# Kernel optimization log

Hardware: AMD Instinct MI355X
Metric: run time of the kernel (lower is better)

The kernel has to match this reference:

```python
import jax, jax.numpy as jnp
import numpy as np

E = 64      # encoding_size (hard-coded in MatchingNetwork)
K = 5       # processing_steps


def _cell(x, h, c, Wih, Whh, bih, bhh):
    # PyTorch LSTMCell: gates ordered i, f, g, o
    z = x @ Wih.T + h @ Whh.T + bih + bhh
    i, f, g, o = jnp.split(z, 4, axis=-1)
    c2 = jax.nn.sigmoid(f) * c + jax.nn.sigmoid(i) * jnp.tanh(g)
    h2 = jax.nn.sigmoid(o) * jnp.tanh(c2)
    return h2, c2


def _lstm_seq(xs, Wih, Whh, bih, bhh, reverse=False):
    # xs: [B, S, E] -> per-step hidden states [B, S, E]
    B = xs.shape[0]
    xs_t = jnp.swapaxes(xs, 0, 1)  # [S, B, E]
    if reverse:
        xs_t = xs_t[::-1]
    h0 = jnp.zeros((B, Wih.shape[0] // 4), xs.dtype)

    def step(carry, x_t):
        h, c = carry
        h2, c2 = _cell(x_t, h, c, Wih, Whh, bih, bhh)
        return (h2, c2), h2

    _, hs = jax.lax.scan(step, (h0, h0), xs_t)
    if reverse:
        hs = hs[::-1]
    return jnp.swapaxes(hs, 0, 1)


def setup_inputs() -> dict:
    key = jax.random.key(0)
    ks = jax.random.split(key, 16)
    B, N, k, T, L, V = 64, 20, 10, 128, 40, 32000
    support_tokens = jax.random.randint(ks[0], (B, N, k, L), 0, V)
    target_tokens = jax.random.randint(ks[1], (B, T, L), 0, V)
    emb = jax.random.normal(ks[2], (V, E), jnp.float32) * 0.1
    emb = emb.at[0].set(0.0)  # padding_idx row
    s = 1.0 / np.sqrt(E)

    def lstm_params(k1, k2, k3, k4):
        return (jax.random.uniform(k1, (4 * E, E), jnp.float32, -s, s),
                jax.random.uniform(k2, (4 * E, E), jnp.float32, -s, s),
                jax.random.uniform(k3, (4 * E,), jnp.float32, -s, s),
                jax.random.uniform(k4, (4 * E,), jnp.float32, -s, s))

    f_Wih, f_Whh, f_bih, f_bhh = lstm_params(ks[3], ks[4], ks[5], ks[6])
    gf_Wih, gf_Whh, gf_bih, gf_bhh = lstm_params(ks[7], ks[8], ks[9], ks[10])
    gb_Wih, gb_Whh, gb_bih, gb_bhh = lstm_params(ks[11], ks[12], ks[13], ks[14])
    return {
        'support_tokens': support_tokens, 'target_tokens': target_tokens,
        'emb': emb,
        'f_Wih': f_Wih, 'f_Whh': f_Whh, 'f_bih': f_bih, 'f_bhh': f_bhh,
        'gf_Wih': gf_Wih, 'gf_Whh': gf_Whh, 'gf_bih': gf_bih, 'gf_bhh': gf_bhh,
        'gb_Wih': gb_Wih, 'gb_Whh': gb_Whh, 'gb_bih': gb_bih, 'gb_bhh': gb_bhh,
    }


def reference(support_tokens, target_tokens, emb,
              f_Wih, f_Whh, f_bih, f_bhh,
              gf_Wih, gf_Whh, gf_bih, gf_bhh,
              gb_Wih, gb_Whh, gb_bih, gb_bhh):
    B, N, kk, L = support_tokens.shape
    T = target_tokens.shape[1]

    # EncodingLayer: embedding lookup + sum-pool over sentence length
    sup_enc = emb[support_tokens].sum(axis=3)   # [B, N, k, E]
    tgt_enc = emb[target_tokens].sum(axis=2)    # [B, T, E]

    # GLayer: bidirectional LSTM over flattened support, sum dirs + residual
    flat = sup_enc.reshape(B, N * kk, E)
    hf = _lstm_seq(flat, gf_Wih, gf_Whh, gf_bih, gf_bhh, reverse=False)
    hb = _lstm_seq(flat, gb_Wih, gb_Whh, gb_bih, gb_bhh, reverse=True)
    sup_emb = (hf + hb).reshape(B, N, kk, E) + sup_enc  # [B, N, k, E]

    # FLayer: K-step attention LSTM over targets
    x = tgt_enc.reshape(B * T, E)
    h = jnp.zeros_like(x)
    c = jnp.zeros_like(x)
    r = jnp.zeros_like(x)
    for _ in range(K):
        h = h + r
        h_next, c = _cell(x, h, c, f_Wih, f_Whh, f_bih, f_bhh)
        h_next = h_next + x
        scores = jnp.einsum('bte,bnke->btnk', h.reshape(B, T, E), sup_emb)
        att = jax.nn.softmax(scores.reshape(B, T, N * kk), axis=2).reshape(B, T, N, kk)
        r = jnp.einsum('btnk,bnke->bte', att, sup_emb).reshape(B * T, E)
        h = h_next
    tgt_emb = h.reshape(B, T, E)

    # Cosine-similarity attention over support set (softmax over N*k)
    num = jnp.einsum('bte,bnke->btnk', tgt_emb, sup_emb)
    tn = jnp.linalg.norm(tgt_emb, axis=-1)          # [B, T]
    sn = jnp.linalg.norm(sup_emb, axis=-1)          # [B, N, k]
    sims = num / jnp.maximum(tn[:, :, None, None] * sn[:, None, :, :], 1e-8)
    attention = jax.nn.softmax(sims.reshape(B, T, N * kk), axis=2).reshape(B, T, N, kk)
    return attention
```

## Files before the change

kernel.cpp:

```cpp
#include <hip/hip_runtime.h>

#define Bn   64
#define Tn   128
#define NKn  200
#define En   64
#define Ln   40

__device__ __forceinline__ float sigm_f(float x){ return 1.0f/(1.0f+__expf(-x)); }
__device__ __forceinline__ float tanh_f(float x){ float e=__expf(2.0f*x); return 1.0f-2.0f/(e+1.0f); }
__device__ __forceinline__ float rdl(float v, int ln){
  return __uint_as_float(__builtin_amdgcn_readlane(__float_as_uint(v), (unsigned)ln));
}

__global__ __launch_bounds__(256) void embed_all(const int* __restrict__ sup,
                                                 const int* __restrict__ tgt,
                                                 const float* __restrict__ emb,
                                                 float* __restrict__ sup_enc,
                                                 float* __restrict__ tgt_enc){
  int tid = threadIdx.x;
  int gr  = blockIdx.x*16 + (tid>>4);
  int e4  = tid & 15;
  const int* tr; float* out;
  if (gr < 12800){ tr = sup + (size_t)gr*Ln;        out = sup_enc + (size_t)gr*64; }
  else           { int r2=gr-12800; tr = tgt + (size_t)r2*Ln; out = tgt_enc + (size_t)r2*64; }
  float4 acc = {0.f,0.f,0.f,0.f};
  #pragma unroll 4
  for (int t=0;t<Ln;t++){
    int tok = tr[t];
    float4 v = ((const float4*)emb)[(size_t)tok*16 + e4];
    acc.x+=v.x; acc.y+=v.y; acc.z+=v.z; acc.w+=v.w;
  }
  ((float4*)out)[e4] = acc;
}

__global__ __launch_bounds__(256,1) void gemm_sup2(const float* __restrict__ x,
                                                   const float* __restrict__ Wa, const float* __restrict__ Wb,
                                                   const float* __restrict__ ba1,const float* __restrict__ ba2,
                                                   const float* __restrict__ bb1,const float* __restrict__ bb2,
                                                   float* __restrict__ outa, float* __restrict__ outb){
  int tid=threadIdx.x, l=tid&63, w=tid>>6;
  int g=tid;
  int m0 = blockIdx.x*16;
  __shared__ __attribute__((aligned(16))) float xs[16*64];
  #pragma unroll
  for(int q=0;q<4;q++){ int r=4*w+q; xs[r*64+l]=x[(size_t)(m0+r)*64+l]; }
  float wa[64], wb[64];
  {
    const float4* A4=(const float4*)(Wa + (size_t)g*64);
    const float4* B4=(const float4*)(Wb + (size_t)g*64);
    #pragma unroll
    for(int q=0;q<16;q++){
      float4 va=A4[q]; wa[4*q]=va.x; wa[4*q+1]=va.y; wa[4*q+2]=va.z; wa[4*q+3]=va.w;
      float4 vb=B4[q]; wb[4*q]=vb.x; wb[4*q+1]=vb.y; wb[4*q+2]=vb.z; wb[4*q+3]=vb.w;
    }
  }
  float biasa=ba1[g]+ba2[g], biasb=bb1[g]+bb2[g];
  __syncthreads();
  #pragma unroll
  for(int r=0;r<16;r++){
    const float4* x4=(const float4*)&xs[r*64];
    float a0=biasa,a1=0.f,b0=biasb,b1=0.f;
    #pragma unroll
    for(int kc=0;kc<16;kc++){
      float4 h4=x4[kc];
      a0=fmaf(wa[4*kc+0],h4.x,a0); b0=fmaf(wb[4*kc+0],h4.x,b0);
      a1=fmaf(wa[4*kc+1],h4.y,a1); b1=fmaf(wb[4*kc+1],h4.y,b1);
      a0=fmaf(wa[4*kc+2],h4.z,a0); b0=fmaf(wb[4*kc+2],h4.z,b0);
      a1=fmaf(wa[4*kc+3],h4.w,a1); b1=fmaf(wb[4*kc+3],h4.w,b1);
    }
    outa[(size_t)(m0+r)*256+g]=a0+a1;
    outb[(size_t)(m0+r)*256+g]=b0+b1;
  }
}

__global__ __launch_bounds__(512,2) void lstm_fb(const float* __restrict__ xg_f,
                                                 const float* __restrict__ xg_b,
                                                 const float* __restrict__ Whh_f,
                                                 const float* __restrict__ Whh_b,
                                                 float* __restrict__ hf,
                                                 float* __restrict__ hb){
  int tid=threadIdx.x, l=tid&63;
  int wl=(tid>>6)&3;
  int chain=tid>>8;
  int b=blockIdx.x;
  const float* xg = chain? xg_b : xg_f;
  const float* Whh= chain? Whh_b: Whh_f;
  float* out      = chain? hb : hf;
  int g=wl*64+l;
  float wr[64];
  {
    const float4* W4=(const float4*)(Whh+(size_t)g*64);
    #pragma unroll
    for(int q=0;q<16;q++){ float4 v=W4[q]; wr[4*q]=v.x; wr[4*q+1]=v.y; wr[4*q+2]=v.z; wr[4*q+3]=v.w; }
  }
  __shared__ float z_s[2][2][256];
  float h=0.f, c=0.f;
  const int tstart = chain?(NKn-1):0, dt = chain?-1:1;
  const float* xgb = xg + (size_t)b*NKn*256 + g;
  float xv0 = xgb[(size_t)tstart*256];
  float xv1 = xgb[(size_t)(tstart+dt)*256];
  for(int s=0;s<NKn;s++){
    int t=tstart+s*dt;
    float xnx=0.f;
    if (s+2<NKn) xnx = xgb[(size_t)(t+2*dt)*256];
    float a0=xv0,a1=0.f,a2=0.f,a3=0.f;
    #pragma unroll
    for(int q=0;q<16;q++){
      a0=fmaf(wr[4*q+0],rdl(h,4*q+0),a0);
      a1=fmaf(wr[4*q+1],rdl(h,4*q+1),a1);
      a2=fmaf(wr[4*q+2],rdl(h,4*q+2),a2);
      a3=fmaf(wr[4*q+3],rdl(h,4*q+3),a3);
    }
    int p=s&1;
    z_s[p][chain][g]=(a0+a1)+(a2+a3);
    __syncthreads();
    float zi=z_s[p][chain][l], zf=z_s[p][chain][64+l],
          zg2=z_s[p][chain][128+l], zo=z_s[p][chain][192+l];
    c = sigm_f(zf)*c + sigm_f(zi)*tanh_f(zg2);
    h = sigm_f(zo)*tanh_f(c);
    if(wl==0) out[((size_t)b*NKn+t)*64+l]=h;
    xv0=xv1; xv1=xnx;
  }
}

__global__ __launch_bounds__(256,2) void gemmz_combine(const float* __restrict__ tgt_enc,
                                                       const float* __restrict__ W,
                                                       const float* __restrict__ b1,
                                                       const float* __restrict__ b2,
                                                       float* __restrict__ zx,
                                                       const float* __restrict__ hf,
                                                       const float* __restrict__ hb,
                                                       const float* __restrict__ sup_enc,
                                                       float* __restrict__ semb,
                                                       float* __restrict__ sn){
  int tid=threadIdx.x, l=tid&63, w=tid>>6;
  int blk=blockIdx.x;
  if (blk < 512){
    int g=tid, m0=blk*16;
    __shared__ __attribute__((aligned(16))) float xs[16*64];
    #pragma unroll
    for(int q=0;q<4;q++){ int r=4*w+q; xs[r*64+l]=tgt_enc[(size_t)(m0+r)*64+l]; }
    float wr[64];
    const float4* W4=(const float4*)(W + (size_t)g*64);
    #pragma unroll
    for(int q=0;q<16;q++){ float4 v=W4[q]; wr[4*q]=v.x; wr[4*q+1]=v.y; wr[4*q+2]=v.z; wr[4*q+3]=v.w; }
    float bias=b1[g]+b2[g];
    __syncthreads();
    #pragma unroll
    for(int r=0;r<16;r++){
      const float4* x4=(const float4*)&xs[r*64];
      float a0=bias,a1=0.f,a2=0.f,a3=0.f;
      #pragma unroll
      for(int kc=0;kc<16;kc++){
        float4 h4=x4[kc];
        a0=fmaf(wr[4*kc+0],h4.x,a0);
        a1=fmaf(wr[4*kc+1],h4.y,a1);
        a2=fmaf(wr[4*kc+2],h4.z,a2);
        a3=fmaf(wr[4*kc+3],h4.w,a3);
      }
      zx[(size_t)(m0+r)*256+g]=(a0+a1)+(a2+a3);
    }
  } else {
    int m0=(blk-512)*16;
    #pragma unroll
    for(int q=0;q<4;q++){
      size_t m=(size_t)m0 + w*4 + q;
      float v = hf[m*64+l] + hb[m*64+l] + sup_enc[m*64+l];
      semb[m*64+l]=v;
      float s=v*v;
      #pragma unroll
      for (int o=32;o>0;o>>=1) s += __shfl_xor(s,o,64);
      if (l==0) sn[m]=sqrtf(s);
    }
  }
}

__global__ __launch_bounds__(256,1) void fused_K(const float* __restrict__ zx,
                                                 const float* __restrict__ Whh,
                                                 const float* __restrict__ x,
                                                 const float* __restrict__ semb,
                                                 const float* __restrict__ sn,
                                                 float* __restrict__ out){
  int tid=threadIdx.x, l=tid&63, w=tid>>6;
  int b=blockIdx.x>>3, t0=(blockIdx.x&7)*16;
  int m0=b*Tn+t0;
  int g=tid;
  bool valid = g<NKn;
  const float* sbase = semb + (size_t)b*NKn*64;
  __shared__ __attribute__((aligned(16))) float hu_s[16*64];
  __shared__ __attribute__((aligned(16))) float sbuf[16*256];
  __shared__ __attribute__((aligned(16))) float hn_s[16*64];
  __shared__ float wredA[64], wredB[64];
  float wr[64], s4f[64];
  {
    const float4* W4=(const float4*)(Whh+(size_t)g*64);
    #pragma unroll
    for(int q=0;q<16;q++){ float4 v=W4[q]; wr[4*q]=v.x; wr[4*q+1]=v.y; wr[4*q+2]=v.z; wr[4*q+3]=v.w; }
  }
  if(valid){
    const float4* sp=(const float4*)(sbase+(size_t)g*64);
    #pragma unroll
    for(int q=0;q<16;q++){ float4 v=sp[q]; s4f[4*q]=v.x; s4f[4*q+1]=v.y; s4f[4*q+2]=v.z; s4f[4*q+3]=v.w; }
  } else {
    #pragma unroll
    for(int q=0;q<64;q++) s4f[q]=0.f;
  }
  float zxr[16];
  #pragma unroll
  for(int r=0;r<16;r++) zxr[r]=zx[(size_t)(m0+r)*256+g];
  float xr[4];
  #pragma unroll
  for(int q=0;q<4;q++) xr[q]=x[(size_t)(m0+q*4+w)*64+l];
  float snr = valid ? sn[(size_t)b*NKn+g] : 1.f;
  float cq[4]={0.f,0.f,0.f,0.f};
  float scr[16], ex[16], mx[16];
  for(int k=0;k<5;k++){
    if(k==0){
      #pragma unroll
      for(int r=0;r<16;r++){ sbuf[r*256+g]=zxr[r]; scr[r]=0.f; }
    } else {
      #pragma unroll
      for(int r=0;r<16;r++){
        float z0=zxr[r], z1=0.f, sc0=0.f, sc1=0.f;
        const float4* h4p=(const float4*)&hu_s[r*64];
        #pragma unroll
        for(int kc=0;kc<16;kc++){
          float4 h4=h4p[kc];
          z0 =fmaf(wr[4*kc+0] ,h4.x,z0 ); sc0=fmaf(s4f[4*kc+0],h4.x,sc0);
          z1 =fmaf(wr[4*kc+1] ,h4.y,z1 ); sc1=fmaf(s4f[4*kc+1],h4.y,sc1);
          z0 =fmaf(wr[4*kc+2] ,h4.z,z0 ); sc0=fmaf(s4f[4*kc+2],h4.z,sc0);
          z1 =fmaf(wr[4*kc+3] ,h4.w,z1 ); sc1=fmaf(s4f[4*kc+3],h4.w,sc1);
        }
        sbuf[r*256+g]=z0+z1;
        scr[r]=sc0+sc1;
      }
    }
    __syncthreads();
    #pragma unroll
    for(int q=0;q<4;q++){
      int r=q*4+w;
      float zi=sbuf[r*256+l], zf=sbuf[r*256+64+l], zg=sbuf[r*256+128+l], zo=sbuf[r*256+192+l];
      float c=sigm_f(zf)*cq[q]+sigm_f(zi)*tanh_f(zg);
      cq[q]=c;
      hn_s[r*64+l]=sigm_f(zo)*tanh_f(c)+xr[q];
    }
    if(k<4){
      #pragma unroll
      for(int t=0;t<16;t++){
        float m = valid ? scr[t] : -1e30f;
        #pragma unroll
        for(int o=32;o>0;o>>=1) m=fmaxf(m,__shfl_xor(m,o,64));
        mx[t]=m;
      }
      if(l==0){
        #pragma unroll
        for(int t=0;t<16;t++) wredA[t*4+w]=mx[t];
      }
      __syncthreads();
      #pragma unroll
      for(int t=0;t<16;t++){
        const float4 m4=*(const float4*)&wredA[t*4];
        float gm=fmaxf(fmaxf(m4.x,m4.y),fmaxf(m4.z,m4.w));
        float e=valid?__expf(scr[t]-gm):0.f;
        ex[t]=e;
        float s=e;
        #pragma unroll
        for(int o=32;o>0;o>>=1) s+=__shfl_xor(s,o,64);
        mx[t]=s;
      }
      if(l==0){
        #pragma unroll
        for(int t=0;t<16;t++) wredB[t*4+w]=mx[t];
      }
      __syncthreads();
      #pragma unroll
      for(int t=0;t<16;t++){
        const float4 s4v=*(const float4*)&wredB[t*4];
        float tot=(s4v.x+s4v.y)+(s4v.z+s4v.w);
        ex[t]*=1.0f/tot;
      }
      if(valid){
        #pragma unroll
        for(int cg=0;cg<4;cg++)
          *(float4*)&sbuf[g*20+4*cg]=make_float4(ex[4*cg+0],ex[4*cg+1],ex[4*cg+2],ex[4*cg+3]);
      }
      __syncthreads();
      float r0=0.f,r1=0.f,r2=0.f,r3=0.f;
      #pragma unroll 8
      for(int j=0;j<NKn;j++){
        float4 a4=*(const float4*)&sbuf[j*20+w*4];
        float sv=sbase[(size_t)j*64+l];
        r0=fmaf(a4.x,sv,r0);
        r1=fmaf(a4.y,sv,r1);
        r2=fmaf(a4.z,sv,r2);
        r3=fmaf(a4.w,sv,r3);
      }
      int rb=w*4;
      hu_s[(rb+0)*64+l]=r0 + hn_s[(rb+0)*64+l];
      hu_s[(rb+1)*64+l]=r1 + hn_s[(rb+1)*64+l];
      hu_s[(rb+2)*64+l]=r2 + hn_s[(rb+2)*64+l];
      hu_s[(rb+3)*64+l]=r3 + hn_s[(rb+3)*64+l];
      __syncthreads();
    }
  }
  __syncthreads();
  float tnorm[16];
  #pragma unroll
  for(int t=0;t<16;t++){
    float v=hn_s[t*64+l];
    float s=v*v;
    #pragma unroll
    for(int o=32;o>0;o>>=1) s+=__shfl_xor(s,o,64);
    tnorm[t]=sqrtf(s);
  }
  #pragma unroll
  for(int t=0;t<16;t++){
    const float4* h4p=(const float4*)&hn_s[t*64];
    float a0=0.f,a1=0.f;
    #pragma unroll
    for(int kc=0;kc<16;kc++){
      float4 h4=h4p[kc];
      a0=fmaf(s4f[4*kc+0],h4.x,a0);
      a1=fmaf(s4f[4*kc+1],h4.y,a1);
      a0=fmaf(s4f[4*kc+2],h4.z,a0);
      a1=fmaf(s4f[4*kc+3],h4.w,a1);
    }
    scr[t]=(a0+a1) / fmaxf(tnorm[t]*snr,1e-8f);
  }
  #pragma unroll
  for(int t=0;t<16;t++){
    float m = valid ? scr[t] : -1e30f;
    #pragma unroll
    for(int o=32;o>0;o>>=1) m=fmaxf(m,__shfl_xor(m,o,64));
    mx[t]=m;
  }
  if(l==0){
    #pragma unroll
    for(int t=0;t<16;t++) wredA[t*4+w]=mx[t];
  }
  __syncthreads();
  #pragma unroll
  for(int t=0;t<16;t++){
    const float4 m4=*(const float4*)&wredA[t*4];
    float gm=fmaxf(fmaxf(m4.x,m4.y),fmaxf(m4.z,m4.w));
    float e=valid?__expf(scr[t]-gm):0.f;
    ex[t]=e;
    float s=e;
    #pragma unroll
    for(int o=32;o>0;o>>=1) s+=__shfl_xor(s,o,64);
    mx[t]=s;
  }
  if(l==0){
    #pragma unroll
    for(int t=0;t<16;t++) wredB[t*4+w]=mx[t];
  }
  __syncthreads();
  #pragma unroll
  for(int t=0;t<16;t++){
    const float4 s4v=*(const float4*)&wredB[t*4];
    float tot=(s4v.x+s4v.y)+(s4v.z+s4v.w);
    if(valid) out[((size_t)(m0+t))*NKn + g]=ex[t]*(1.0f/tot);
  }
}

extern "C" void kernel_launch(void* const* d_in, const int* in_sizes, int n_in,
                              void* d_out, int out_size, void* d_ws, size_t ws_size,
                              hipStream_t stream) {
  (void)in_sizes; (void)n_in; (void)out_size; (void)ws_size;
  const int*   sup_toks = (const int*)d_in[0];
  const int*   tgt_toks = (const int*)d_in[1];
  const float* emb      = (const float*)d_in[2];
  const float* f_Wih    = (const float*)d_in[3];
  const float* f_Whh    = (const float*)d_in[4];
  const float* f_bih    = (const float*)d_in[5];
  const float* f_bhh    = (const float*)d_in[6];
  const float* gf_Wih   = (const float*)d_in[7];
  const float* gf_Whh   = (const float*)d_in[8];
  const float* gf_bih   = (const float*)d_in[9];
  const float* gf_bhh   = (const float*)d_in[10];
  const float* gb_Wih   = (const float*)d_in[11];
  const float* gb_Whh   = (const float*)d_in[12];
  const float* gb_bih   = (const float*)d_in[13];
  const float* gb_bhh   = (const float*)d_in[14];

  float* ws = (float*)d_ws;
  float* sup_enc = ws;
  float* tgt_enc = sup_enc + 819200;
  float* bufA    = tgt_enc + 524288;
  float* bufB    = bufA    + 3276800;
  float* semb    = bufB    + 3276800;
  float* hb      = semb    + 819200;
  float* sn      = hb      + 819200;

  float* xg_f = bufA;
  float* xg_b = bufB;

  embed_all<<<1312,256,0,stream>>>(sup_toks, tgt_toks, emb, sup_enc, tgt_enc);
  gemm_sup2<<<800,256,0,stream>>>(sup_enc, gf_Wih, gb_Wih,
                                  gf_bih, gf_bhh, gb_bih, gb_bhh, xg_f, xg_b);
  lstm_fb<<<64,512,0,stream>>>(xg_f, xg_b, gf_Whh, gb_Whh, semb , hb);

  float* zx = bufA;

  gemmz_combine<<<1312,256,0,stream>>>(tgt_enc, f_Wih, f_bih, f_bhh, zx,
                                       semb, hb, sup_enc, semb, sn);

  fused_K<<<512,256,0,stream>>>(zx, f_Whh, tgt_enc, semb, sn, (float*)d_out);
}
```

Baseline: 422.2 us.

## Split bidirectional LSTM across blocks and K-dimension halves to shorten per-step chain

The recurrent support LSTM now uses 128 blocks, one per (direction, batch), instead of 64 blocks that each held both directions. Within a block, each gate row's 64-term recurrent dot product is split across two thread halves that combine partial sums through shared memory, which halves the serial FMA/readlane chain per step. Input-gate preloads are batched eight steps ahead, and hidden states are buffered in LDS and written out once at the end rather than every step. The cost is extra shared-memory traffic per step and a larger LDS footprint.

```diff
diff --git a/kernel.cpp b/kernel.cpp
--- a/kernel.cpp
+++ b/kernel.cpp
@@ -73,53 +73,69 @@
   }
 }
 
-__global__ __launch_bounds__(512,2) void lstm_fb(const float* __restrict__ xg_f,
-                                                 const float* __restrict__ xg_b,
-                                                 const float* __restrict__ Whh_f,
-                                                 const float* __restrict__ Whh_b,
-                                                 float* __restrict__ hf,
-                                                 float* __restrict__ hb){
+__global__ __launch_bounds__(512,1) void lstm_split(const float* __restrict__ xg_f,
+                                                    const float* __restrict__ xg_b,
+                                                    const float* __restrict__ Whh_f,
+                                                    const float* __restrict__ Whh_b,
+                                                    float* __restrict__ hf,
+                                                    float* __restrict__ hb){
   int tid=threadIdx.x, l=tid&63;
-  int wl=(tid>>6)&3;
-  int chain=tid>>8;
-  int b=blockIdx.x;
-  const float* xg = chain? xg_b : xg_f;
-  const float* Whh= chain? Whh_b: Whh_f;
-  float* out      = chain? hb : hf;
-  int g=wl*64+l;
-  float wr[64];
+  int g=tid&255;
+  int half=tid>>8;
+  int dir=blockIdx.x>>6, b=blockIdx.x&63;
+  const float* xg = dir? xg_b : xg_f;
+  const float* Whh= dir? Whh_b: Whh_f;
+  float* out      = dir? hb : hf;
+  float wr[32];
   {
-    const float4* W4=(const float4*)(Whh+(size_t)g*64);
-    #pragma unroll
-    for(int q=0;q<16;q++){ float4 v=W4[q]; wr[4*q]=v.x; wr[4*q+1]=v.y; wr[4*q+2]=v.z; wr[4*q+3]=v.w; }
-  }
-  __shared__ float z_s[2][2][256];
+    const float4* W4=(const float4*)(Whh+(size_t)g*64+half*32);
+    #pragma unroll
+    for(int q=0;q<8;q++){ float4 v=W4[q]; wr[4*q]=v.x; wr[4*q+1]=v.y; wr[4*q+2]=v.z; wr[4*q+3]=v.w; }
+  }
+  __shared__ float zp[2][256][2];
+  __shared__ float hh[NKn*64];
   float h=0.f, c=0.f;
-  const int tstart = chain?(NKn-1):0, dt = chain?-1:1;
+  const int tstart = dir?(NKn-1):0, dt = dir?-1:1;
   const float* xgb = xg + (size_t)b*NKn*256 + g;
-  float xv0 = xgb[(size_t)tstart*256];
-  float xv1 = xgb[(size_t)(tstart+dt)*256];
+  float xq[8], xnq[8];
+  if(half==0){
+    #pragma unroll
+    for(int j=0;j<8;j++) xq[j]=xgb[(size_t)(tstart+j*dt)*256];
+    #pragma unroll
+    for(int j=0;j<8;j++) xnq[j]=0.f;
+  }
+  const int kbase = half*32;
   for(int s=0;s<NKn;s++){
-    int t=tstart+s*dt;
-    float xnx=0.f;
-    if (s+2<NKn) xnx = xgb[(size_t)(t+2*dt)*256];
-    float a0=xv0,a1=0.f,a2=0.f,a3=0.f;
-    #pragma unroll
-    for(int q=0;q<16;q++){
-      a0=fmaf(wr[4*q+0],rdl(h,4*q+0),a0);
-      a1=fmaf(wr[4*q+1],rdl(h,4*q+1),a1);
-      a2=fmaf(wr[4*q+2],rdl(h,4*q+2),a2);
-      a3=fmaf(wr[4*q+3],rdl(h,4*q+3),a3);
+    float a0 = (half==0)? xq[s&7] : 0.f;
+    float a1 = 0.f;
+    #pragma unroll
+    for(int k=0;k<32;k+=2){
+      a0=fmaf(wr[k]  ,rdl(h,kbase+k  ),a0);
+      a1=fmaf(wr[k+1],rdl(h,kbase+k+1),a1);
     }
     int p=s&1;
-    z_s[p][chain][g]=(a0+a1)+(a2+a3);
+    zp[p][g][half]=a0+a1;
     __syncthreads();
-    float zi=z_s[p][chain][l], zf=z_s[p][chain][64+l],
-          zg2=z_s[p][chain][128+l], zo=z_s[p][chain][192+l];
+    if (half==0 && (s&7)==0 && s+8<NKn){
+      #pragma unroll
+      for(int j=0;j<8;j++) xnq[j]=xgb[(size_t)(tstart+(s+8+j)*dt)*256];
+    }
+    const float2* zr=(const float2*)&zp[p][0][0];
+    float2 vi=zr[l], vf=zr[64+l], vg=zr[128+l], vo=zr[192+l];
+    float zi=vi.x+vi.y, zf=vf.x+vf.y, zg2=vg.x+vg.y, zo=vo.x+vo.y;
     c = sigm_f(zf)*c + sigm_f(zi)*tanh_f(zg2);
     h = sigm_f(zo)*tanh_f(c);
-    if(wl==0) out[((size_t)b*NKn+t)*64+l]=h;
-    xv0=xv1; xv1=xnx;
+    if(tid<64) hh[s*64+l]=h;
+    if (half==0 && (s&7)==7){
+      #pragma unroll
+      for(int j=0;j<8;j++) xq[j]=xnq[j];
+    }
+  }
+  __syncthreads();
+  for(int i=tid;i<NKn*64;i+=512){
+    int t=i>>6, e=i&63;
+    int s = dir? (NKn-1-t) : t;
+    out[((size_t)b*NKn+t)*64+e] = hh[s*64+e];
   }
 }
 
@@ -398,7 +414,7 @@
   embed_all<<<1312,256,0,stream>>>(sup_toks, tgt_toks, emb, sup_enc, tgt_enc);
   gemm_sup2<<<800,256,0,stream>>>(sup_enc, gf_Wih, gb_Wih,
                                   gf_bih, gf_bhh, gb_bih, gb_bhh, xg_f, xg_b);
-  lstm_fb<<<64,512,0,stream>>>(xg_f, xg_b, gf_Whh, gb_Whh, semb , hb);
+  lstm_split<<<128,512,0,stream>>>(xg_f, xg_b, gf_Whh, gb_Whh, semb , hb);
 
   float* zx = bufA;
 
```

Result: slower. 457.1 us (+8.3%).

## Split bidirectional LSTM into per-direction blocks and fuse input GEMM into attention kernel

Applied to the files above, without the earlier changes.

The bidirectional LSTM now runs as 128 blocks of 256 threads, one direction and batch per block, instead of 64 blocks that each hold both directions. This spreads the serial recurrence over more CUs and leaves each block with a private barrier. The target input projection (Wih·x + bias) moves out of the combine kernel and into the start of the K-step attention kernel. That removes the zx round trip through global memory, and the combine kernel now only builds the support embeddings and their norms. The cost is extra register pressure in fused_K2 from the temporary Wih row, plus a shallower prefetch in the LSTM.

```diff
diff --git a/kernel.cpp b/kernel.cpp
--- a/kernel.cpp
+++ b/kernel.cpp
@@ -73,37 +73,31 @@
   }
 }
 
-__global__ __launch_bounds__(512,2) void lstm_fb(const float* __restrict__ xg_f,
-                                                 const float* __restrict__ xg_b,
-                                                 const float* __restrict__ Whh_f,
-                                                 const float* __restrict__ Whh_b,
-                                                 float* __restrict__ hf,
-                                                 float* __restrict__ hb){
-  int tid=threadIdx.x, l=tid&63;
-  int wl=(tid>>6)&3;
-  int chain=tid>>8;
-  int b=blockIdx.x;
-  const float* xg = chain? xg_b : xg_f;
-  const float* Whh= chain? Whh_b: Whh_f;
-  float* out      = chain? hb : hf;
-  int g=wl*64+l;
+__global__ __launch_bounds__(256,1) void lstm_seq(const float* __restrict__ xg_f,
+                                                  const float* __restrict__ xg_b,
+                                                  const float* __restrict__ Whh_f,
+                                                  const float* __restrict__ Whh_b,
+                                                  float* __restrict__ hf,
+                                                  float* __restrict__ hb){
+  int tid=threadIdx.x, l=tid&63, w=tid>>6;
+  int dir=blockIdx.x>>6, b=blockIdx.x&63;
+  const float* xg = dir? xg_b : xg_f;
+  const float* Whh= dir? Whh_b: Whh_f;
+  float* out = dir? hb : hf;
   float wr[64];
-  {
-    const float4* W4=(const float4*)(Whh+(size_t)g*64);
-    #pragma unroll
-    for(int q=0;q<16;q++){ float4 v=W4[q]; wr[4*q]=v.x; wr[4*q+1]=v.y; wr[4*q+2]=v.z; wr[4*q+3]=v.w; }
-  }
-  __shared__ float z_s[2][2][256];
+  const float4* W4=(const float4*)(Whh+(size_t)(w*64+l)*64);
+  #pragma unroll
+  for(int q=0;q<16;q++){ float4 v=W4[q]; wr[4*q]=v.x; wr[4*q+1]=v.y; wr[4*q+2]=v.z; wr[4*q+3]=v.w; }
+  __shared__ float z_s[2][256];
   float h=0.f, c=0.f;
-  const int tstart = chain?(NKn-1):0, dt = chain?-1:1;
-  const float* xgb = xg + (size_t)b*NKn*256 + g;
-  float xv0 = xgb[(size_t)tstart*256];
-  float xv1 = xgb[(size_t)(tstart+dt)*256];
+  const int tstart = dir?(NKn-1):0, dt = dir?-1:1;
+  const float* xgb = xg + (size_t)b*NKn*256 + w*64 + l;
+  float xv = xgb[(size_t)tstart*256];
   for(int s=0;s<NKn;s++){
     int t=tstart+s*dt;
     float xnx=0.f;
-    if (s+2<NKn) xnx = xgb[(size_t)(t+2*dt)*256];
-    float a0=xv0,a1=0.f,a2=0.f,a3=0.f;
+    if (s<NKn-1) xnx = xgb[(size_t)(t+dt)*256];
+    float a0=xv,a1=0.f,a2=0.f,a3=0.f;
     #pragma unroll
     for(int q=0;q<16;q++){
       a0=fmaf(wr[4*q+0],rdl(h,4*q+0),a0);
@@ -111,76 +105,43 @@
       a2=fmaf(wr[4*q+2],rdl(h,4*q+2),a2);
       a3=fmaf(wr[4*q+3],rdl(h,4*q+3),a3);
     }
-    int p=s&1;
-    z_s[p][chain][g]=(a0+a1)+(a2+a3);
+    z_s[s&1][tid]=(a0+a1)+(a2+a3);
     __syncthreads();
-    float zi=z_s[p][chain][l], zf=z_s[p][chain][64+l],
-          zg2=z_s[p][chain][128+l], zo=z_s[p][chain][192+l];
-    c = sigm_f(zf)*c + sigm_f(zi)*tanh_f(zg2);
+    float zi=z_s[s&1][l], zf=z_s[s&1][64+l], zg=z_s[s&1][128+l], zo=z_s[s&1][192+l];
+    c = sigm_f(zf)*c + sigm_f(zi)*tanh_f(zg);
     h = sigm_f(zo)*tanh_f(c);
-    if(wl==0) out[((size_t)b*NKn+t)*64+l]=h;
-    xv0=xv1; xv1=xnx;
-  }
-}
-
-__global__ __launch_bounds__(256,2) void gemmz_combine(const float* __restrict__ tgt_enc,
-                                                       const float* __restrict__ W,
-                                                       const float* __restrict__ b1,
-                                                       const float* __restrict__ b2,
-                                                       float* __restrict__ zx,
-                                                       const float* __restrict__ hf,
-                                                       const float* __restrict__ hb,
-                                                       const float* __restrict__ sup_enc,
-                                                       float* __restrict__ semb,
-                                                       float* __restrict__ sn){
+    if(w==0) out[((size_t)b*NKn+t)*64+l]=h;
+    xv=xnx;
+  }
+}
+
+__global__ __launch_bounds__(256,2) void combine(const float* __restrict__ hf,
+                                                 const float* __restrict__ hb,
+                                                 const float* __restrict__ sup_enc,
+                                                 float* __restrict__ semb,
+                                                 float* __restrict__ sn){
   int tid=threadIdx.x, l=tid&63, w=tid>>6;
-  int blk=blockIdx.x;
-  if (blk < 512){
-    int g=tid, m0=blk*16;
-    __shared__ __attribute__((aligned(16))) float xs[16*64];
-    #pragma unroll
-    for(int q=0;q<4;q++){ int r=4*w+q; xs[r*64+l]=tgt_enc[(size_t)(m0+r)*64+l]; }
-    float wr[64];
-    const float4* W4=(const float4*)(W + (size_t)g*64);
-    #pragma unroll
-    for(int q=0;q<16;q++){ float4 v=W4[q]; wr[4*q]=v.x; wr[4*q+1]=v.y; wr[4*q+2]=v.z; wr[4*q+3]=v.w; }
-    float bias=b1[g]+b2[g];
-    __syncthreads();
-    #pragma unroll
-    for(int r=0;r<16;r++){
-      const float4* x4=(const float4*)&xs[r*64];
-      float a0=bias,a1=0.f,a2=0.f,a3=0.f;
-      #pragma unroll
-      for(int kc=0;kc<16;kc++){
-        float4 h4=x4[kc];
-        a0=fmaf(wr[4*kc+0],h4.x,a0);
-        a1=fmaf(wr[4*kc+1],h4.y,a1);
-        a2=fmaf(wr[4*kc+2],h4.z,a2);
-        a3=fmaf(wr[4*kc+3],h4.w,a3);
-      }
-      zx[(size_t)(m0+r)*256+g]=(a0+a1)+(a2+a3);
-    }
-  } else {
-    int m0=(blk-512)*16;
-    #pragma unroll
-    for(int q=0;q<4;q++){
-      size_t m=(size_t)m0 + w*4 + q;
-      float v = hf[m*64+l] + hb[m*64+l] + sup_enc[m*64+l];
-      semb[m*64+l]=v;
-      float s=v*v;
-      #pragma unroll
-      for (int o=32;o>0;o>>=1) s += __shfl_xor(s,o,64);
-      if (l==0) sn[m]=sqrtf(s);
-    }
-  }
-}
-
-__global__ __launch_bounds__(256,1) void fused_K(const float* __restrict__ zx,
-                                                 const float* __restrict__ Whh,
-                                                 const float* __restrict__ x,
-                                                 const float* __restrict__ semb,
-                                                 const float* __restrict__ sn,
-                                                 float* __restrict__ out){
+  int m0=blockIdx.x*16;
+  #pragma unroll
+  for(int q=0;q<4;q++){
+    size_t m=(size_t)m0 + w*4 + q;
+    float v = hf[m*64+l] + hb[m*64+l] + sup_enc[m*64+l];
+    semb[m*64+l]=v;
+    float s=v*v;
+    #pragma unroll
+    for (int o=32;o>0;o>>=1) s += __shfl_xor(s,o,64);
+    if (l==0) sn[m]=sqrtf(s);
+  }
+}
+
+__global__ __launch_bounds__(256,1) void fused_K2(const float* __restrict__ tgt_enc,
+                                                  const float* __restrict__ Wih,
+                                                  const float* __restrict__ bih,
+                                                  const float* __restrict__ bhh,
+                                                  const float* __restrict__ Whh,
+                                                  const float* __restrict__ semb,
+                                                  const float* __restrict__ sn,
+                                                  float* __restrict__ out){
   int tid=threadIdx.x, l=tid&63, w=tid>>6;
   int b=blockIdx.x>>3, t0=(blockIdx.x&7)*16;
   int m0=b*Tn+t0;
@@ -191,6 +152,34 @@
   __shared__ __attribute__((aligned(16))) float sbuf[16*256];
   __shared__ __attribute__((aligned(16))) float hn_s[16*64];
   __shared__ float wredA[64], wredB[64];
+  #pragma unroll
+  for(int q=0;q<4;q++){ int r=4*w+q; hu_s[r*64+l]=tgt_enc[(size_t)(m0+r)*64+l]; }
+  float zxr[16];
+  {
+    float wih[64];
+    const float4* W4=(const float4*)(Wih+(size_t)g*64);
+    #pragma unroll
+    for(int q=0;q<16;q++){ float4 v=W4[q]; wih[4*q]=v.x; wih[4*q+1]=v.y; wih[4*q+2]=v.z; wih[4*q+3]=v.w; }
+    float bias=bih[g]+bhh[g];
+    __syncthreads();
+    #pragma unroll
+    for(int r=0;r<16;r++){
+      const float4* x4=(const float4*)&hu_s[r*64];
+      float a0=bias,a1=0.f,a2=0.f,a3=0.f;
+      #pragma unroll
+      for(int kc=0;kc<16;kc++){
+        float4 h4=x4[kc];
+        a0=fmaf(wih[4*kc+0],h4.x,a0);
+        a1=fmaf(wih[4*kc+1],h4.y,a1);
+        a2=fmaf(wih[4*kc+2],h4.z,a2);
+        a3=fmaf(wih[4*kc+3],h4.w,a3);
+      }
+      zxr[r]=(a0+a1)+(a2+a3);
+    }
+  }
+  float xr[4];
+  #pragma unroll
+  for(int q=0;q<4;q++) xr[q]=hu_s[(q*4+w)*64+l];
   float wr[64], s4f[64];
   {
     const float4* W4=(const float4*)(Whh+(size_t)g*64);
@@ -205,12 +194,6 @@
     #pragma unroll
     for(int q=0;q<64;q++) s4f[q]=0.f;
   }
-  float zxr[16];
-  #pragma unroll
-  for(int r=0;r<16;r++) zxr[r]=zx[(size_t)(m0+r)*256+g];
-  float xr[4];
-  #pragma unroll
-  for(int q=0;q<4;q++) xr[q]=x[(size_t)(m0+q*4+w)*64+l];
   float snr = valid ? sn[(size_t)b*NKn+g] : 1.f;
   float cq[4]={0.f,0.f,0.f,0.f};
   float scr[16], ex[16], mx[16];
@@ -398,12 +381,8 @@
   embed_all<<<1312,256,0,stream>>>(sup_toks, tgt_toks, emb, sup_enc, tgt_enc);
   gemm_sup2<<<800,256,0,stream>>>(sup_enc, gf_Wih, gb_Wih,
                                   gf_bih, gf_bhh, gb_bih, gb_bhh, xg_f, xg_b);
-  lstm_fb<<<64,512,0,stream>>>(xg_f, xg_b, gf_Whh, gb_Whh, semb , hb);
-
-  float* zx = bufA;
-
-  gemmz_combine<<<1312,256,0,stream>>>(tgt_enc, f_Wih, f_bih, f_bhh, zx,
-                                       semb, hb, sup_enc, semb, sn);
-
-  fused_K<<<512,256,0,stream>>>(zx, f_Whh, tgt_enc, semb, sn, (float*)d_out);
-}
+  lstm_seq<<<128,256,0,stream>>>(xg_f, xg_b, gf_Whh, gb_Whh, semb , hb);
+  combine<<<800,256,0,stream>>>(semb, hb, sup_enc, semb, sn);
+  fused_K2<<<512,256,0,stream>>>(tgt_enc, f_Wih, f_bih, f_bhh, f_Whh,
+                                 semb, sn, (float*)d_out);
+}
```

Result: slower. 638.1 us (+51.1%).
